# Optimization experiments

Measured on AMD Instinct MI355X. Metric: run time of the kernel, lower is better.

## Reference

```python
import jax, jax.numpy as jnp
import numpy as np
import math

D_MODEL = 1024
N_HEADS = 16
D_HEAD = D_MODEL // N_HEADS
D_FF = 4096
BATCH = 2
SEQ = 2048
EPS = 1e-5


def _rmsnorm(x, w):
    rms = jnp.sqrt(jnp.mean(x * x, axis=-1, keepdims=True) + EPS)
    return (x / rms) * w


def _gelu_erf(x):
    # matches 0.5 * x * (1 + erf(x / sqrt(2)))
    return 0.5 * x * (1.0 + jax.lax.erf(x / jnp.sqrt(jnp.asarray(2.0, x.dtype))))


def setup_inputs() -> dict:
    key = jax.random.key(0)
    ks = jax.random.split(key, 6)
    scale = 0.02
    x = jax.random.normal(ks[0], (BATCH, SEQ, D_MODEL), dtype=jnp.float32)
    w_qkv = jax.random.normal(ks[1], (3 * D_MODEL, D_MODEL), dtype=jnp.float32) * scale
    w_o = jax.random.normal(ks[2], (D_MODEL, D_MODEL), dtype=jnp.float32) * scale
    ln1_w = jnp.ones((D_MODEL,), dtype=jnp.float32)
    ln2_w = jnp.ones((D_MODEL,), dtype=jnp.float32)
    w1 = jax.random.normal(ks[3], (D_FF, D_MODEL), dtype=jnp.float32) * scale
    w2 = jax.random.normal(ks[4], (D_MODEL, D_FF), dtype=jnp.float32) * scale
    return {"x": x, "w_qkv": w_qkv, "w_o": w_o, "ln1_w": ln1_w,
            "ln2_w": ln2_w, "w1": w1, "w2": w2}


def reference(x, w_qkv, w_o, ln1_w, ln2_w, w1, w2):
    B, S, D = x.shape
    # --- attention sublayer (pre-norm) ---
    h = _rmsnorm(x, ln1_w)
    qkv = jnp.einsum('bsd,ed->bse', h, w_qkv)            # (B,S,3*D)
    qkv = qkv.reshape(B, S, 3, N_HEADS, D_HEAD)
    q, k, v = jnp.moveaxis(qkv, 2, 0)                    # each (B,S,H,dh)
    q = q.transpose(0, 2, 1, 3)                          # (B,H,S,dh)
    k = k.transpose(0, 2, 1, 3)
    v = v.transpose(0, 2, 1, 3)
    scores = jnp.einsum('bhqd,bhkd->bhqk', q, k) / math.sqrt(D_HEAD)
    causal = jnp.tril(jnp.ones((S, S), dtype=bool))      # True = keep
    scores = jnp.where(causal, scores, jnp.asarray(-jnp.inf, scores.dtype))
    attn = jax.nn.softmax(scores, axis=-1)
    ctx = jnp.einsum('bhqk,bhkd->bhqd', attn, v)         # (B,H,S,dh)
    ctx = ctx.transpose(0, 2, 1, 3).reshape(B, S, D)
    attn_out = jnp.einsum('bsd,ed->bse', ctx, w_o)
    first_sum = x + attn_out
    # --- FFN sublayer (pre-norm) ---
    h2 = _rmsnorm(first_sum, ln2_w)
    ff = jnp.einsum('bsf,df->bsd', _gelu_erf(jnp.einsum('bsd,fd->bsf', h2, w1)), w2)
    return first_sum + ff
```

## Files before the change

kernel.cpp:

```cpp
#include <hip/hip_runtime.h>

typedef unsigned short u16;
typedef unsigned int u32;
typedef __attribute__((ext_vector_type(8))) short short8;
typedef __attribute__((ext_vector_type(4))) float f32x4;

#define AS1 __attribute__((address_space(1)))
#define AS3 __attribute__((address_space(3)))

__device__ __forceinline__ u16 f2bf(float f) {
  union { float f; unsigned u; } v; v.f = f;
  return (u16)((v.u + 0x7fffu + ((v.u >> 16) & 1u)) >> 16);
}
__device__ __forceinline__ u32 pack2bf(float a, float b) {
  return (u32)f2bf(a) | ((u32)f2bf(b) << 16);
}
__device__ __forceinline__ float bf2f(u16 h) {
  union { u32 u; float f; } v; v.u = ((u32)h) << 16; return v.f;
}
__device__ __forceinline__ u32 permpack(float a, float b) {
  union { float f; u32 u; } ua, ub; ua.f = a; ub.f = b;
  return __builtin_amdgcn_perm(ub.u, ua.u, 0x07060302u);
}


__global__ __launch_bounds__(256)
void packb_kernel(const float* __restrict__ wqkv, const float* __restrict__ wo,
                  const float* __restrict__ w1, const float* __restrict__ w2,
                  u16* __restrict__ oqkv, u16* __restrict__ oo,
                  u16* __restrict__ o1, u16* __restrict__ o2) {
  __shared__ u16 Ls[128][40];
  const int b = blockIdx.x, t = threadIdx.x;
  const float* W; u16* O; int nb, kb, KB; float scale = 1.0f;
  if (b < 768)       { W = wqkv; O = oqkv; KB = 32;  int i2 = b;        nb = i2 >> 5; kb = i2 & 31;
                       if (nb >= 8 && nb < 16) scale = 0.125f; }
  else if (b < 1024) { W = wo;   O = oo;   KB = 32;  int i2 = b - 768;  nb = i2 >> 5; kb = i2 & 31; }
  else if (b < 2048) { W = w1;   O = o1;   KB = 32;  int i2 = b - 1024; nb = i2 >> 5; kb = i2 & 31; }
  else               { W = w2;   O = o2;   KB = 128; int i2 = b - 2048; nb = i2 >> 7; kb = i2 & 127; }
  const int K = KB * 32;
  {
    const int r = t >> 1, c0 = (t & 1) * 16;
    const float* src = W + (size_t)(nb * 128 + r) * K + kb * 32 + c0;
#pragma unroll
    for (int e = 0; e < 16; ++e) Ls[r][c0 + e] = f2bf(src[e] * scale);
  }
  __syncthreads();
  const int f = t >> 5, l0 = (t & 31) * 2;
  u16* dst = O + ((size_t)(nb * KB + kb) * 8 + f) * 512 + (size_t)l0 * 8;
  short8 v0, v1;
#pragma unroll
  for (int e = 0; e < 8; ++e) v0[e] = (short)Ls[f * 16 + (l0 & 15)][(l0 >> 4) * 8 + e];
  const int l1 = l0 + 1;
#pragma unroll
  for (int e = 0; e < 8; ++e) v1[e] = (short)Ls[f * 16 + (l1 & 15)][(l1 >> 4) * 8 + e];
  *(short8*)dst = v0;
  *(short8*)(dst + 8) = v1;
}

__global__ void rmsnorm_kernel(const float* __restrict__ x, const float* __restrict__ w,
                               u16* __restrict__ out) {
  const int row = blockIdx.x, tid = threadIdx.x;
  const float4 v = ((const float4*)(x + (size_t)row * 1024))[tid];
  float ss = v.x * v.x + v.y * v.y + v.z * v.z + v.w * v.w;
#pragma unroll
  for (int off = 32; off > 0; off >>= 1) ss += __shfl_xor(ss, off);
  __shared__ float red[4];
  if ((tid & 63) == 0) red[tid >> 6] = ss;
  __syncthreads();
  float tot = red[0] + red[1] + red[2] + red[3];
  float scale = 1.0f / sqrtf(tot * (1.0f / 1024.0f) + 1e-5f);
  const float4 wv = ((const float4*)w)[tid];
  const int kb = tid >> 3, quadp = (tid >> 1) & 3, e0 = (tid & 1) * 4;
  const int mb = row >> 7, i_o = (row >> 4) & 7, l16_o = row & 15;
  size_t off = (((size_t)mb * 32 + kb) * 8 + i_o) * 512 + (quadp * 16 + l16_o) * 8 + e0;
  u32 lo = pack2bf(v.x * scale * wv.x, v.y * scale * wv.y);
  u32 hi = pack2bf(v.z * scale * wv.z, v.w * scale * wv.w);
  *(uint2*)(out + off) = make_uint2(lo, hi);
}

template <int EPI>
__global__ __launch_bounds__(256, 3)
void gemm_pp(const u16* __restrict__ Ap, const u16* __restrict__ Bp,
             const float* __restrict__ RES, void* __restrict__ OUT,
             int M, int N, int K, int KS) {
  const int tid = threadIdx.x;
  const int wave = tid >> 6, lane = tid & 63;
  const int quad = lane >> 4, l16 = lane & 15;
  int bx = blockIdx.x, by = blockIdx.y;
  const int gx = gridDim.x, gy = gridDim.y;
  if (((gx & 1) | (gy & 3)) == 0) {
    const int lin = blockIdx.x + gx * blockIdx.y;
    const int xcd = lin & 7, j = lin >> 3;
    const int rw = gx >> 1;
    bx = (xcd & 1) * rw + j % rw;
    by = (xcd >> 1) * (gy >> 2) + j / rw;
  }
  const int wm = (wave >> 1) * 64, wn = (wave & 1) * 64;
  const int KB = K >> 5;
  f32x4 acc[4][4] = {};

  const int kb0 = (blockIdx.z * KS) >> 5;
  const int nkb = KS >> 5;
  const u16* Aw = Ap + (((size_t)by * KB + kb0) * 8 + (wm >> 4)) * 512 + (size_t)lane * 8;
  const u16* Bw = Bp + (((size_t)bx * KB + kb0) * 8 + (wn >> 4)) * 512 + (size_t)lane * 8;

  short8 af[4], bfc[4];
#pragma unroll
  for (int j = 0; j < 4; ++j) {
    af[j]  = *(const short8*)(Aw + j * 512);
    bfc[j] = *(const short8*)(Bw + j * 512);
  }
  for (int it = 0; it < nkb - 1; ++it) {
    Aw += 4096; Bw += 4096;
    short8 an[4], bn[4];
#pragma unroll
    for (int j = 0; j < 4; ++j) {
      an[j] = *(const short8*)(Aw + j * 512);
      bn[j] = *(const short8*)(Bw + j * 512);
    }
#pragma unroll
    for (int i = 0; i < 4; ++i)
#pragma unroll
      for (int j = 0; j < 4; ++j)
        acc[i][j] = __builtin_amdgcn_mfma_f32_16x16x32_bf16(af[i], bfc[j], acc[i][j], 0, 0, 0);
#pragma unroll
    for (int j = 0; j < 4; ++j) { af[j] = an[j]; bfc[j] = bn[j]; }
  }
#pragma unroll
  for (int i = 0; i < 4; ++i)
#pragma unroll
    for (int j = 0; j < 4; ++j)
      acc[i][j] = __builtin_amdgcn_mfma_f32_16x16x32_bf16(af[i], bfc[j], acc[i][j], 0, 0, 0);

  const int m0 = by * 128, n0 = bx * 128;
  const size_t zoff = (size_t)blockIdx.z * M * N;
#pragma unroll
  for (int i = 0; i < 4; ++i) {
#pragma unroll
    for (int j = 0; j < 4; ++j) {
#pragma unroll
      for (int r = 0; r < 4; ++r) {
        int row = m0 + wm + i * 16 + quad * 4 + r;
        int col = n0 + wn + j * 16 + l16;
        size_t idx = (size_t)row * N + col;
        float v = acc[i][j][r];
        if constexpr (EPI == 0) {
          ((u16*)OUT)[idx] = f2bf(v);
        } else if constexpr (EPI == 1) {
          ((float*)OUT)[idx] = RES[idx] + v;
        } else if constexpr (EPI == 2) {
          float g = 0.5f * v * (1.0f + erff(v * 0.70710678118654752f));
          const int kb_o = col >> 5, quadp = (col >> 3) & 3, e = col & 7;
          const int mb_o = row >> 7, i_o = (row >> 4) & 7, l16_o = row & 15;
          size_t off = (((size_t)mb_o * (N >> 5) + kb_o) * 8 + i_o) * 512
                       + (quadp * 16 + l16_o) * 8 + e;
          ((u16*)OUT)[off] = f2bf(g);
        } else {
          ((u16*)OUT)[zoff + idx] = f2bf(v);
        }
      }
    }
  }
}

__global__ void reduce4_kernel(const float* __restrict__ fs,
                               const u16* __restrict__ P,
                               float* __restrict__ out, size_t n) {
  size_t i = ((size_t)blockIdx.x * 256 + threadIdx.x) * 4;
  float4 a = *(const float4*)(fs + i);
  float s[4] = {a.x, a.y, a.z, a.w};
#pragma unroll
  for (int z = 0; z < 4; ++z) {
    ushort4 q = *(const ushort4*)(P + z * n + i);
    s[0] += bf2f(q.x); s[1] += bf2f(q.y); s[2] += bf2f(q.z); s[3] += bf2f(q.w);
  }
  *(float4*)(out + i) = make_float4(s[0], s[1], s[2], s[3]);
}

__global__ __launch_bounds__(256)
void packkv_kernel(const u16* __restrict__ qkv, u16* __restrict__ Kp,
                   u16* __restrict__ Vp) {
  __shared__ __align__(16) u16 Ks[32][72];
  __shared__ __align__(16) u16 Vs[32][72];
  const int kt = blockIdx.x, h = blockIdx.y, b = blockIdx.z;
  const int tid = threadIdx.x;
  const int key0 = kt * 32;
  {
    const size_t g = (size_t)b * 2048 * 3072 + (size_t)(key0 + (tid >> 3)) * 3072
                     + h * 64 + (tid & 7) * 8;
    *(short8*)(&Ks[tid >> 3][(tid & 7) * 8]) = *(const short8*)(qkv + g + 1024);
    *(short8*)(&Vs[tid >> 3][(tid & 7) * 8]) = *(const short8*)(qkv + g + 2048);
  }
  __syncthreads();
  const int wave = tid >> 6, lane = tid & 63;
  const int quad = lane >> 4, l16 = lane & 15;
  const int permrow = 8 * (l16 >> 2) + (l16 & 3);
  const size_t obase = ((size_t)((b * 16 + h) * 64 + kt)) * 2048 + tid * 8;
  {
    int row = permrow + (wave >> 1) * 4;
    int col = quad * 8 + (wave & 1) * 32;
    *(short8*)(Kp + obase) = *(const short8*)(&Ks[row][col]);
  }
  {
    short8 v;
    int col = wave * 16 + l16;
#pragma unroll
    for (int j = 0; j < 8; ++j) v[j] = (short)Vs[quad * 8 + j][col];
    *(short8*)(Vp + obase) = v;
  }
}

struct AttnState {
  f32x4 o0, o1, o2, o3;
  float ls;
};

template <bool MASKED>
__device__ __forceinline__ void attn_tile(
    AttnState& st, const u16* kp, const u16* vp, int key0, int q_abs, int quad,
    short8 qf0, short8 qf1) {
  short8 kf00 = *(const short8*)kp;
  short8 kf01 = *(const short8*)(kp + 512);
  short8 kf10 = *(const short8*)(kp + 1024);
  short8 kf11 = *(const short8*)(kp + 1536);
  short8 vf0 = *(const short8*)vp;
  short8 vf1 = *(const short8*)(vp + 512);
  short8 vf2 = *(const short8*)(vp + 1024);
  short8 vf3 = *(const short8*)(vp + 1536);

  f32x4 s0 = {}, s1 = {};
  s0 = __builtin_amdgcn_mfma_f32_16x16x32_bf16(kf00, qf0, s0, 0, 0, 0);
  s0 = __builtin_amdgcn_mfma_f32_16x16x32_bf16(kf01, qf1, s0, 0, 0, 0);
  s1 = __builtin_amdgcn_mfma_f32_16x16x32_bf16(kf10, qf0, s1, 0, 0, 0);
  s1 = __builtin_amdgcn_mfma_f32_16x16x32_bf16(kf11, qf1, s1, 0, 0, 0);

  float p[8];
#pragma unroll
  for (int r = 0; r < 4; ++r) {
    p[r]     = __expf(s0[r]);
    p[4 + r] = __expf(s1[r]);
  }
  if constexpr (MASKED) {
    const int kb = key0 + 8 * quad;
#pragma unroll
    for (int r = 0; r < 4; ++r) {
      if (kb + r > q_abs)     p[r] = 0.f;
      if (kb + 4 + r > q_abs) p[4 + r] = 0.f;
    }
  }
  st.ls += ((p[0] + p[1]) + (p[2] + p[3])) + ((p[4] + p[5]) + (p[6] + p[7]));

  union { u32 u[4]; short8 s; } pu;
  pu.u[0] = permpack(p[0], p[1]);
  pu.u[1] = permpack(p[2], p[3]);
  pu.u[2] = permpack(p[4], p[5]);
  pu.u[3] = permpack(p[6], p[7]);

  st.o0 = __builtin_amdgcn_mfma_f32_16x16x32_bf16(vf0, pu.s, st.o0, 0, 0, 0);
  st.o1 = __builtin_amdgcn_mfma_f32_16x16x32_bf16(vf1, pu.s, st.o1, 0, 0, 0);
  st.o2 = __builtin_amdgcn_mfma_f32_16x16x32_bf16(vf2, pu.s, st.o2, 0, 0, 0);
  st.o3 = __builtin_amdgcn_mfma_f32_16x16x32_bf16(vf3, pu.s, st.o3, 0, 0, 0);
}

__global__ __launch_bounds__(256)
void attn_kernel(const u16* __restrict__ qkv, const u16* __restrict__ Kpack,
                 const u16* __restrict__ Vpack, u16* __restrict__ ctx) {
  const int bx = blockIdx.x, by = blockIdx.y, bz = blockIdx.z;
  const int h = by, b = bz;
  const int qt = ((by >> 3) & 1) ? (31 - bx) : bx;
  const int tid = threadIdx.x, wave = tid >> 6, lane = tid & 63;
  const int quad = lane >> 4, l16 = lane & 15;
  const int q0 = qt * 64;
  const int qrow = q0 + wave * 16;
  const int q_abs = qrow + l16;
  const size_t base = (size_t)b * 2048 * 3072;
  const size_t headoff = (size_t)((b * 16 + h) * 64) * 2048;
  const u16* Kb = Kpack + headoff + lane * 8;
  const u16* Vb = Vpack + headoff + lane * 8;

  short8 qf0, qf1;
  {
    const u16* qp = qkv + base + (size_t)q_abs * 3072 + h * 64 + quad * 8;
    qf0 = *(const short8*)qp;
    qf1 = *(const short8*)(qp + 32);
  }
  AttnState st;
  st.o0 = f32x4{}; st.o1 = f32x4{}; st.o2 = f32x4{}; st.o3 = f32x4{};
  st.ls = 0.f;

  const int nfull = qrow >> 5;
  for (int kt = 0; kt < nfull; ++kt)
    attn_tile<false>(st, Kb + kt * 2048, Vb + kt * 2048, kt * 32, q_abs, quad, qf0, qf1);
  attn_tile<true>(st, Kb + nfull * 2048, Vb + nfull * 2048, nfull * 32, q_abs, quad, qf0, qf1);

  float ls = st.ls;
  ls += __shfl_xor(ls, 16);
  ls += __shfl_xor(ls, 32);
  float inv = 1.0f / ls;

  const int rgl = b * 2048 + q_abs;
  const int mb = rgl >> 7, i_o = (rgl >> 4) & 7;
  f32x4 o[4] = {st.o0, st.o1, st.o2, st.o3};
#pragma unroll
  for (int c = 0; c < 4; ++c) {
    const int c0 = h * 64 + c * 16 + quad * 4;
    const int kb = c0 >> 5, quadp = (c0 >> 3) & 3, e0 = c0 & 7;
    size_t off = (((size_t)mb * 32 + kb) * 8 + i_o) * 512 + (quadp * 16 + l16) * 8 + e0;
    u32 lo = pack2bf(o[c][0] * inv, o[c][1] * inv);
    u32 hi = pack2bf(o[c][2] * inv, o[c][3] * inv);
    *(uint2*)(ctx + off) = make_uint2(lo, hi);
  }
}

extern "C" void kernel_launch(void* const* d_in, const int* in_sizes, int n_in,
                              void* d_out, int out_size, void* d_ws, size_t ws_size,
                              hipStream_t stream) {
  const float* x     = (const float*)d_in[0];
  const float* w_qkv = (const float*)d_in[1];
  const float* w_o   = (const float*)d_in[2];
  const float* ln1   = (const float*)d_in[3];
  const float* ln2   = (const float*)d_in[4];
  const float* w1    = (const float*)d_in[5];
  const float* w2    = (const float*)d_in[6];
  float* out = (float*)d_out;

  char* p = (char*)d_ws;
  u16* wqkv_b = (u16*)p; p += (size_t)3072 * 1024 * 2;
  u16* wo_b   = (u16*)p; p += (size_t)1024 * 1024 * 2;
  u16* w1_b   = (u16*)p; p += (size_t)4096 * 1024 * 2;
  u16* w2_b   = (u16*)p; p += (size_t)1024 * 4096 * 2;
  u16* h_b    = (u16*)p; p += (size_t)4096 * 1024 * 2;
  u16* qkv_b  = (u16*)p;
  u16* g_b    = qkv_b;
  p += (size_t)4096 * 3072 * 2;
  u16* ctx_b  = (u16*)p; p += (size_t)4096 * 1024 * 2;
  float* fs   = (float*)p; p += (size_t)4096 * 1024 * 4;
  u16* kp_b   = (u16*)fs;
  u16* vp_b   = (u16*)fs + (size_t)4 * 1024 * 1024;
  u16* Pbuf = (u16*)p;
  const size_t need = (size_t)(p - (char*)d_ws) + (size_t)4 * 4096 * 1024 * 2;
  const bool splitk = ws_size >= need;

  packb_kernel<<<3072, 256, 0, stream>>>(w_qkv, w_o, w1, w2,
                                         wqkv_b, wo_b, w1_b, w2_b);

  rmsnorm_kernel<<<4096, 256, 0, stream>>>(x, ln1, h_b);
  gemm_pp<0><<<dim3(24, 32, 1), 256, 0, stream>>>(h_b, wqkv_b, nullptr, qkv_b, 4096, 3072, 1024, 1024);
  packkv_kernel<<<dim3(64, 16, 2), 256, 0, stream>>>(qkv_b, kp_b, vp_b);
  attn_kernel<<<dim3(32, 16, 2), 256, 0, stream>>>(qkv_b, kp_b, vp_b, ctx_b);
  gemm_pp<1><<<dim3(8, 32, 1), 256, 0, stream>>>(ctx_b, wo_b, x, fs, 4096, 1024, 1024, 1024);
  rmsnorm_kernel<<<4096, 256, 0, stream>>>(fs, ln2, h_b);
  gemm_pp<2><<<dim3(32, 32, 1), 256, 0, stream>>>(h_b, w1_b, nullptr, g_b, 4096, 4096, 1024, 1024);
  if (splitk) {
    gemm_pp<3><<<dim3(8, 32, 4), 256, 0, stream>>>(g_b, w2_b, nullptr, Pbuf, 4096, 1024, 4096, 1024);
    reduce4_kernel<<<4096, 256, 0, stream>>>(fs, Pbuf, out, (size_t)4096 * 1024);
  } else {
    gemm_pp<1><<<dim3(8, 32, 1), 256, 0, stream>>>(g_b, w2_b, fs, out, 4096, 1024, 4096, 4096);
  }
}
```

Before: 326.6 us.

## Stage GEMM A tiles in double-buffered LDS via global_load_lds

The packed-bf16 GEMM now copies the A operand into a two-stage shared-memory buffer with async global-to-LDS loads. Waves that share the same rows read A from LDS instead of each fetching it from global memory, which halves A global traffic per block. B fragments are still loaded straight into registers, now prefetched two k-steps at a time. The cost is one block-wide barrier per 64-wide k step plus added LDS use, which may lower occupancy. Correctness also depends on the async LDS writes having finished before the barrier, and on KS being a multiple of 64.

```diff
diff --git a/kernel.cpp b/kernel.cpp
--- a/kernel.cpp
+++ b/kernel.cpp
@@ -83,6 +83,7 @@
 void gemm_pp(const u16* __restrict__ Ap, const u16* __restrict__ Bp,
              const float* __restrict__ RES, void* __restrict__ OUT,
              int M, int N, int K, int KS) {
+  __shared__ __align__(16) u16 As[2][8192];
   const int tid = threadIdx.x;
   const int wave = tid >> 6, lane = tid & 63;
   const int quad = lane >> 4, l16 = lane & 15;
@@ -100,37 +101,59 @@
   f32x4 acc[4][4] = {};
 
   const int kb0 = (blockIdx.z * KS) >> 5;
-  const int nkb = KS >> 5;
-  const u16* Aw = Ap + (((size_t)by * KB + kb0) * 8 + (wm >> 4)) * 512 + (size_t)lane * 8;
+  const int nit = KS >> 6;
+  const u16* Ag = Ap + ((size_t)by * KB + kb0) * 4096 + wave * 2048 + lane * 8;
   const u16* Bw = Bp + (((size_t)bx * KB + kb0) * 8 + (wn >> 4)) * 512 + (size_t)lane * 8;
 
-  short8 af[4], bfc[4];
+  auto stage = [&](int it, int pp) {
+    const u16* s = Ag + (size_t)it * 8192;
+    u16* d = &As[pp][wave * 2048];
+    __builtin_amdgcn_global_load_lds((AS1 void*)s, (AS3 void*)d, 16, 0, 0);
+    __builtin_amdgcn_global_load_lds((AS1 void*)(s + 512), (AS3 void*)(d + 512), 16, 0, 0);
+    __builtin_amdgcn_global_load_lds((AS1 void*)(s + 1024), (AS3 void*)(d + 1024), 16, 0, 0);
+    __builtin_amdgcn_global_load_lds((AS1 void*)(s + 1536), (AS3 void*)(d + 1536), 16, 0, 0);
+  };
+
+  stage(0, 0);
+  short8 bfr[8];
 #pragma unroll
   for (int j = 0; j < 4; ++j) {
-    af[j]  = *(const short8*)(Aw + j * 512);
-    bfc[j] = *(const short8*)(Bw + j * 512);
-  }
-  for (int it = 0; it < nkb - 1; ++it) {
-    Aw += 4096; Bw += 4096;
-    short8 an[4], bn[4];
-#pragma unroll
-    for (int j = 0; j < 4; ++j) {
-      an[j] = *(const short8*)(Aw + j * 512);
-      bn[j] = *(const short8*)(Bw + j * 512);
-    }
-#pragma unroll
-    for (int i = 0; i < 4; ++i)
-#pragma unroll
-      for (int j = 0; j < 4; ++j)
-        acc[i][j] = __builtin_amdgcn_mfma_f32_16x16x32_bf16(af[i], bfc[j], acc[i][j], 0, 0, 0);
-#pragma unroll
-    for (int j = 0; j < 4; ++j) { af[j] = an[j]; bfc[j] = bn[j]; }
-  }
-#pragma unroll
-  for (int i = 0; i < 4; ++i)
-#pragma unroll
-    for (int j = 0; j < 4; ++j)
-      acc[i][j] = __builtin_amdgcn_mfma_f32_16x16x32_bf16(af[i], bfc[j], acc[i][j], 0, 0, 0);
+    bfr[j]     = *(const short8*)(Bw + j * 512);
+    bfr[4 + j] = *(const short8*)(Bw + 4096 + j * 512);
+  }
+  int p = 0;
+  const int abase = (wm >> 4) * 512;
+  for (int it = 0; it < nit; ++it) {
+    __syncthreads();
+    const bool more = (it + 1 < nit);
+    if (more) stage(it + 1, p ^ 1);
+    short8 bn[8];
+    if (more) {
+      const u16* bp = Bw + (size_t)(it + 1) * 8192;
+#pragma unroll
+      for (int j = 0; j < 4; ++j) {
+        bn[j]     = *(const short8*)(bp + j * 512);
+        bn[4 + j] = *(const short8*)(bp + 4096 + j * 512);
+      }
+    }
+#pragma unroll
+    for (int kk = 0; kk < 2; ++kk) {
+      short8 af[4];
+#pragma unroll
+      for (int i = 0; i < 4; ++i)
+        af[i] = *(const short8*)(&As[p][kk * 4096 + abase + i * 512 + lane * 8]);
+#pragma unroll
+      for (int i = 0; i < 4; ++i)
+#pragma unroll
+        for (int j = 0; j < 4; ++j)
+          acc[i][j] = __builtin_amdgcn_mfma_f32_16x16x32_bf16(af[i], bfr[kk * 4 + j], acc[i][j], 0, 0, 0);
+    }
+    if (more) {
+#pragma unroll
+      for (int j = 0; j < 8; ++j) bfr[j] = bn[j];
+    }
+    p ^= 1;
+  }
 
   const int m0 = by * 128, n0 = bx * 128;
   const size_t zoff = (size_t)blockIdx.z * M * N;
```

Result: no change. 329.3 us (+0.8%).

## Stage A tiles through LDS with async global_load_lds double buffering

Applied to the files above, without the earlier changes.

The GEMM used to have each wave load its A fragments directly from global memory into registers, so the two waves sharing a row block fetched the same data twice. The A tile for each k-step is now copied once per block into a double-buffered LDS array with global_load_lds, and waves read their fragments from LDS. This halves redundant global traffic for A and moves the copy off the register path. In exchange it adds a __syncthreads per iteration and LDS usage, which could hurt the 3-blocks-per-SM occupancy target or add stalls. The buffer being overwritten is protected by that barrier.

```diff
diff --git a/kernel.cpp b/kernel.cpp
--- a/kernel.cpp
+++ b/kernel.cpp
@@ -83,6 +83,7 @@
 void gemm_pp(const u16* __restrict__ Ap, const u16* __restrict__ Bp,
              const float* __restrict__ RES, void* __restrict__ OUT,
              int M, int N, int K, int KS) {
+  __shared__ __align__(16) u16 As[2][4096];
   const int tid = threadIdx.x;
   const int wave = tid >> 6, lane = tid & 63;
   const int quad = lane >> 4, l16 = lane & 15;
@@ -100,37 +101,57 @@
   f32x4 acc[4][4] = {};
 
   const int kb0 = (blockIdx.z * KS) >> 5;
-  const int nkb = KS >> 5;
-  const u16* Aw = Ap + (((size_t)by * KB + kb0) * 8 + (wm >> 4)) * 512 + (size_t)lane * 8;
+  const int nit = KS >> 5;
+  const u16* Ag = Ap + ((size_t)by * KB + kb0) * 4096 + wave * 1024 + lane * 8;
   const u16* Bw = Bp + (((size_t)bx * KB + kb0) * 8 + (wn >> 4)) * 512 + (size_t)lane * 8;
 
-  short8 af[4], bfc[4];
-#pragma unroll
-  for (int j = 0; j < 4; ++j) {
-    af[j]  = *(const short8*)(Aw + j * 512);
-    bfc[j] = *(const short8*)(Bw + j * 512);
-  }
-  for (int it = 0; it < nkb - 1; ++it) {
-    Aw += 4096; Bw += 4096;
-    short8 an[4], bn[4];
-#pragma unroll
-    for (int j = 0; j < 4; ++j) {
-      an[j] = *(const short8*)(Aw + j * 512);
-      bn[j] = *(const short8*)(Bw + j * 512);
+  auto stage = [&](int it, int pp) {
+    const u16* s = Ag + (size_t)it * 4096;
+    u16* d = &As[pp][wave * 1024];
+    __builtin_amdgcn_global_load_lds((AS1 void*)s, (AS3 void*)d, 16, 0, 0);
+    __builtin_amdgcn_global_load_lds((AS1 void*)(s + 512), (AS3 void*)(d + 512), 16, 0, 0);
+  };
+
+  stage(0, 0);
+  short8 bfr[4];
+#pragma unroll
+  for (int j = 0; j < 4; ++j) bfr[j] = *(const short8*)(Bw + j * 512);
+  int p = 0;
+  const int abase = (wm >> 4) * 512;
+  for (int it = 0; it < nit - 1; ++it) {
+    __syncthreads();
+    stage(it + 1, p ^ 1);
+    short8 bn[4];
+    {
+      const u16* bp = Bw + (size_t)(it + 1) * 4096;
+#pragma unroll
+      for (int j = 0; j < 4; ++j) bn[j] = *(const short8*)(bp + j * 512);
     }
+    short8 af[4];
 #pragma unroll
     for (int i = 0; i < 4; ++i)
+      af[i] = *(const short8*)(&As[p][abase + i * 512 + lane * 8]);
+#pragma unroll
+    for (int i = 0; i < 4; ++i)
 #pragma unroll
       for (int j = 0; j < 4; ++j)
-        acc[i][j] = __builtin_amdgcn_mfma_f32_16x16x32_bf16(af[i], bfc[j], acc[i][j], 0, 0, 0);
-#pragma unroll
-    for (int j = 0; j < 4; ++j) { af[j] = an[j]; bfc[j] = bn[j]; }
-  }
-#pragma unroll
-  for (int i = 0; i < 4; ++i)
-#pragma unroll
-    for (int j = 0; j < 4; ++j)
-      acc[i][j] = __builtin_amdgcn_mfma_f32_16x16x32_bf16(af[i], bfc[j], acc[i][j], 0, 0, 0);
+        acc[i][j] = __builtin_amdgcn_mfma_f32_16x16x32_bf16(af[i], bfr[j], acc[i][j], 0, 0, 0);
+#pragma unroll
+    for (int j = 0; j < 4; ++j) bfr[j] = bn[j];
+    p ^= 1;
+  }
+  {
+    __syncthreads();
+    short8 af[4];
+#pragma unroll
+    for (int i = 0; i < 4; ++i)
+      af[i] = *(const short8*)(&As[p][abase + i * 512 + lane * 8]);
+#pragma unroll
+    for (int i = 0; i < 4; ++i)
+#pragma unroll
+      for (int j = 0; j < 4; ++j)
+        acc[i][j] = __builtin_amdgcn_mfma_f32_16x16x32_bf16(af[i], bfr[j], acc[i][j], 0, 0, 0);
+  }
 
   const int m0 = by * 128, n0 = bx * 128;
   const size_t zoff = (size_t)blockIdx.z * M * N;
```

New measurement: 320.0 us. 2.0% less time.
